# Performance work log

Measured on AMD Instinct MI355X. Metric: run time of the kernel, lower is better.

## Reference

```python
import jax, jax.numpy as jnp
import numpy as np

MAX_SENTENCE = 12
HIDDEN = 256
INPUT = 18 * 300
NEG = -9999999.0


def _lstm(xs, Wih, Whh, bih, bhh):
    # xs: [T, B, I] -> hs: [T, B, H] (torch LSTM gate order i,f,g,o)
    B = xs.shape[1]
    H = Whh.shape[1]

    def step(carry, x):
        h, c = carry
        g = x @ Wih.T + h @ Whh.T + bih + bhh
        i, f, gg, o = jnp.split(g, 4, axis=-1)
        c = jax.nn.sigmoid(f) * c + jax.nn.sigmoid(i) * jnp.tanh(gg)
        h = jax.nn.sigmoid(o) * jnp.tanh(c)
        return (h, c), h

    init = (jnp.zeros((B, H), xs.dtype), jnp.zeros((B, H), xs.dtype))
    _, hs = jax.lax.scan(step, init, xs)
    return hs


def setup_inputs() -> dict:
    key = jax.random.key(0)
    ks = jax.random.split(key, 16)
    s = 0.05
    return {
        "x": jax.random.normal(ks[0], (512, MAX_SENTENCE, INPUT), jnp.float32),
        "Wih_f": jax.random.normal(ks[1], (4 * HIDDEN, INPUT), jnp.float32) * s,
        "Whh_f": jax.random.normal(ks[2], (4 * HIDDEN, HIDDEN), jnp.float32) * s,
        "bih_f": jax.random.normal(ks[3], (4 * HIDDEN,), jnp.float32) * s,
        "bhh_f": jax.random.normal(ks[4], (4 * HIDDEN,), jnp.float32) * s,
        "Wih_b": jax.random.normal(ks[5], (4 * HIDDEN, INPUT), jnp.float32) * s,
        "Whh_b": jax.random.normal(ks[6], (4 * HIDDEN, HIDDEN), jnp.float32) * s,
        "bih_b": jax.random.normal(ks[7], (4 * HIDDEN,), jnp.float32) * s,
        "bhh_b": jax.random.normal(ks[8], (4 * HIDDEN,), jnp.float32) * s,
        "enc_W": jax.random.normal(ks[9], (50, 2 * HIDDEN), jnp.float32) * s,
        "enc_b": jax.random.normal(ks[10], (50,), jnp.float32) * s,
        "wfc_W": jax.random.normal(ks[11], (1, 100), jnp.float32) * s,
        "wfc_b": jax.random.normal(ks[12], (1,), jnp.float32) * s,
        "fc_W": jax.random.normal(ks[13], (2, MAX_SENTENCE), jnp.float32) * s,
        "fc_b": jax.random.normal(ks[14], (2,), jnp.float32) * s,
    }


def reference(x, Wih_f, Whh_f, bih_f, bhh_f, Wih_b, Whh_b, bih_b, bhh_b,
              enc_W, enc_b, wfc_W, wfc_b, fc_W, fc_b):
    # Bidirectional LSTM over the document axis (seq-first, batch = MAX_SENTENCE)
    hf = _lstm(x, Wih_f, Whh_f, bih_f, bhh_f)                       # [D, S, H]
    hb = jnp.flip(_lstm(jnp.flip(x, 0), Wih_b, Whh_b, bih_b, bhh_b), 0)
    H = jnp.concatenate([hf, hb], axis=-1)                           # [D, S, 2H]

    # Sentence encoder: Linear(2H,50) + LeakyReLU (dropout = identity, eval)
    enc = jax.nn.leaky_relu(H @ enc_W.T + enc_b, 0.01)               # [D, S, 50]

    # Pairwise affinity Wij[d,i,j] = w_fc(concat(enc_i, enc_j)); split-weight trick
    w1, w2 = wfc_W[0, :50], wfc_W[0, 50:]
    a = enc @ w1                                                     # [D, S]
    b = enc @ w2                                                     # [D, S]
    Wij = a[:, :, None] + b[:, None, :] + wfc_b[0]                   # [D, S, S]
    eye = jnp.eye(MAX_SENTENCE, dtype=bool)
    Wij = jnp.where(eye, NEG, Wij)

    # Core sentence: argmax over off-diagonal row sums
    rowsum = jnp.sum(jnp.where(eye, 0.0, Wij), axis=-1)              # [D, S]
    core = jnp.argmax(rowsum, axis=-1)                               # [D]

    # Cosine similarity of each sentence to the core sentence -> rank scores
    Hn = H / (jnp.linalg.norm(H, axis=-1, keepdims=True) + 1e-12)
    core_vec = jnp.take_along_axis(Hn, core[:, None, None], axis=1)  # [D, 1, 2H]
    sim = jnp.sum(Hn * core_vec, axis=-1)                            # [D, S]
    order = jnp.argsort(-sim, axis=-1)
    ranks = jnp.argsort(order, axis=-1)
    rank_score = 1.0 - ranks.astype(H.dtype) / MAX_SENTENCE          # [D, S]

    # Row-scaled affinities, zero diagonal for aggregation
    Wmask = jnp.where(eye, 0.0, Wij) * rank_score[:, :, None]        # [D, S, S]

    # Two rounds of weighted neighbor aggregation
    emb = H
    for _ in range(2):
        emb = emb + jnp.einsum('dij,djh->dih', Wmask, emb)

    doc = jnp.mean(emb, axis=-1)                                     # [D, S]
    return doc @ fc_W.T + fc_b                                       # [D, 2]
```

## Files before the change

### kernel.cpp

```cpp
#include <hip/hip_runtime.h>
#include <hip/hip_bf16.h>
#include <hip/hip_fp16.h>


typedef _Float16 h8 __attribute__((ext_vector_type(8)));
typedef _Float16 h2 __attribute__((ext_vector_type(2)));
typedef float f4 __attribute__((ext_vector_type(4)));

#define SEQ 512
#define NL 12
#define KIN 5400
#define KP 5408
#define NG 2048
#define MROWS 6144

__device__ __forceinline__ unsigned int pk2(float a, float b){
  h2 v; v[0] = (_Float16)a; v[1] = (_Float16)b;
  return __builtin_bit_cast(unsigned int, v);
}
__device__ __forceinline__ float dot2u(unsigned int h, unsigned int w, float acc){
  return __builtin_amdgcn_fdot2(__builtin_bit_cast(h2, h), __builtin_bit_cast(h2, w), acc, false);
}
__device__ __forceinline__ float sigm(float x){ return 1.f/(1.f + __expf(-x)); }
__device__ __forceinline__ float tanhx(float x){ return 1.f - 2.f/(__expf(2.f*x) + 1.f); }

__global__ void cvt_x(const float* __restrict__ x, _Float16* __restrict__ xh){
  int idx = blockIdx.x * 256 + threadIdx.x;
  int row = idx / KP, col = idx - row * KP;
  float v = (col < KIN) ? x[(size_t)row * KIN + col] : 0.f;
  xh[idx] = (_Float16)v;
}

__global__ void cvt_w(const float* __restrict__ wf, const float* __restrict__ wb,
                      _Float16* __restrict__ wh){
  int idx = blockIdx.x * 256 + threadIdx.x;
  int row = idx / KP, col = idx - row * KP;
  float v = 0.f;
  if (col < KIN)
    v = (row < 1024) ? wf[(size_t)row * KIN + col] : wb[(size_t)(row - 1024) * KIN + col];
  wh[idx] = (_Float16)v;
}

__global__ __launch_bounds__(256) void gemm_in(
    const _Float16* __restrict__ A, const _Float16* __restrict__ B, _Float16* __restrict__ G,
    const float* __restrict__ bif, const float* __restrict__ bhf,
    const float* __restrict__ bib, const float* __restrict__ bhb){
  __shared__ _Float16 As[128 * 40];
  __shared__ _Float16 Bs[128 * 40];
  int tid = threadIdx.x;
  int bm = blockIdx.x % 48, bn = blockIdx.x / 48;
  int wid = tid >> 6, ln = tid & 63;
  int wm = wid & 1, wn = wid >> 1;
  int l15 = ln & 15, q = ln >> 4;
  int i0 = tid, i1 = tid + 256;
  int r0 = i0 >> 2, c0 = i0 & 3, r1 = i1 >> 2, c1 = i1 & 3;
  const size_t a0 = (size_t)(bm*128 + r0) * KP + c0*8;
  const size_t a1 = (size_t)(bm*128 + r1) * KP + c1*8;
  const size_t b0 = (size_t)(bn*128 + r0) * KP + c0*8;
  const size_t b1 = (size_t)(bn*128 + r1) * KP + c1*8;
  f4 acc[4][4] = {};
  for (int kk = 0; kk < 169; ++kk){
    int k0 = kk * 32;
    uint4 va0 = *(const uint4*)(A + a0 + k0);
    uint4 va1 = *(const uint4*)(A + a1 + k0);
    uint4 vb0 = *(const uint4*)(B + b0 + k0);
    uint4 vb1 = *(const uint4*)(B + b1 + k0);
    __syncthreads();
    *(uint4*)(As + r0*40 + c0*8) = va0;
    *(uint4*)(As + r1*40 + c1*8) = va1;
    *(uint4*)(Bs + r0*40 + c0*8) = vb0;
    *(uint4*)(Bs + r1*40 + c1*8) = vb1;
    __syncthreads();
    h8 af[4], bfr[4];
    #pragma unroll
    for (int mt = 0; mt < 4; ++mt)
      af[mt] = *(const h8*)(As + (wm*64 + mt*16 + l15)*40 + q*8);
    #pragma unroll
    for (int nt = 0; nt < 4; ++nt)
      bfr[nt] = *(const h8*)(Bs + (wn*64 + nt*16 + l15)*40 + q*8);
    #pragma unroll
    for (int mt = 0; mt < 4; ++mt)
      #pragma unroll
      for (int nt = 0; nt < 4; ++nt)
        acc[mt][nt] = __builtin_amdgcn_mfma_f32_16x16x32_f16(af[mt], bfr[nt], acc[mt][nt], 0, 0, 0);
  }
  float bias[4];
  #pragma unroll
  for (int nt = 0; nt < 4; ++nt){
    int col = bn*128 + wn*64 + nt*16 + l15;
    bias[nt] = (col < 1024) ? (bif[col] + bhf[col]) : (bib[col-1024] + bhb[col-1024]);
  }
  #pragma unroll
  for (int mt = 0; mt < 4; ++mt)
    #pragma unroll
    for (int nt = 0; nt < 4; ++nt)
      #pragma unroll
      for (int r = 0; r < 4; ++r){
        int row = bm*128 + wm*64 + mt*16 + q*4 + r;
        int col = bn*128 + wn*64 + nt*16 + l15;
        G[(size_t)row * NG + col] = (_Float16)(acc[mt][nt][r] + bias[nt]);
      }
}

__global__ __launch_bounds__(512, 2) void lstm_rec(
    const float* __restrict__ Whhf, const float* __restrict__ Whhb,
    const _Float16* __restrict__ G, float* __restrict__ Hout){
  __shared__ unsigned int tailw[12][1024];
  __shared__ unsigned int hlds[128];
  __shared__ float fg[256], og[256];
  int b = blockIdx.x;
  int dir = b / 12, lane = b - dir * 12;
  int t = threadIdx.x;
  const float* Whh = dir ? Whhb : Whhf;
  int r0 = t, r1 = t + 512;
  unsigned int wa[116], wb[116];
  #pragma unroll
  for (int c = 0; c < 128; ++c){
    float2 v0 = *(const float2*)(Whh + (size_t)r0 * 256 + 2*c);
    float2 v1 = *(const float2*)(Whh + (size_t)r1 * 256 + 2*c);
    unsigned int u0 = pk2(v0.x, v0.y);
    unsigned int u1 = pk2(v1.x, v1.y);
    if (c < 116){ wa[c] = u0; wb[c] = u1; }
    else { tailw[c - 116][r0] = u0; tailw[c - 116][r1] = u1; }
  }
  if (t < 128) hlds[t] = 0u;
  float cst = 0.f;
  __syncthreads();
  for (int it = 0; it < SEQ; ++it){
    int s = dir ? (SEQ - 1 - it) : it;
    const _Float16* gp = G + (size_t)(s*NL + lane) * NG + dir * 1024;
    float ga = (float)gp[r0];
    float gb = (float)gp[r1];
    float acc0 = 0.f, acc1 = 0.f;
    #pragma unroll
    for (int c4 = 0; c4 < 29; ++c4){
      uint4 hq = *(const uint4*)&hlds[c4*4];
      unsigned int ha[4] = {hq.x, hq.y, hq.z, hq.w};
      #pragma unroll
      for (int j = 0; j < 4; ++j){
        acc0 = dot2u(ha[j], wa[c4*4 + j], acc0);
        acc1 = dot2u(ha[j], wb[c4*4 + j], acc1);
      }
    }
    #pragma unroll
    for (int c4 = 0; c4 < 3; ++c4){
      uint4 hq = *(const uint4*)&hlds[116 + c4*4];
      unsigned int ha[4] = {hq.x, hq.y, hq.z, hq.w};
      #pragma unroll
      for (int j = 0; j < 4; ++j){
        int cc = c4*4 + j;
        acc0 = dot2u(ha[j], tailw[cc][r0], acc0);
        acc1 = dot2u(ha[j], tailw[cc][r1], acc1);
      }
    }
    acc0 += ga; acc1 += gb;
    __syncthreads();
    if (t >= 256){ fg[t - 256] = acc0; og[t - 256] = acc1; }
    __syncthreads();
    if (t < 256){
      float iv = acc0, gv = acc1, fv = fg[t], ov = og[t];
      cst = sigm(fv)*cst + sigm(iv)*tanhx(gv);
      float hv = sigm(ov)*tanhx(cst);
      ((_Float16*)hlds)[t] = (_Float16)hv;
      Hout[(size_t)(s*NL + lane)*512 + dir*256 + t] = hv;
    }
    __syncthreads();
  }
}

__global__ __launch_bounds__(256) void epilogue(
    const float* __restrict__ H, const float* __restrict__ encW, const float* __restrict__ encB,
    const float* __restrict__ wfcW, const float* __restrict__ wfcB,
    const float* __restrict__ fcW, const float* __restrict__ fcB, float* __restrict__ out){
  __shared__ float B0[12][516];
  __shared__ float B1[12][516];
  __shared__ float encl[12][52];
  __shared__ float part[12][16];
  __shared__ float av[12], bv[12], nrm[12], simv[12], rsv[12], docv[12];
  __shared__ float Wm[12][12];
  __shared__ int corei;
  int d = blockIdx.x, t = threadIdx.x;
  const float* Hd = H + (size_t)d * NL * 512;
  for (int idx = t; idx < NL * 128; idx += 256){
    int i = idx >> 7, h4 = (idx & 127) * 4;
    *(f4*)(&B0[i][h4]) = *(const f4*)(Hd + i*512 + h4);
  }
  __syncthreads();
  for (int idx = t; idx < 600; idx += 256){
    int i = idx % 12, e = idx / 12;
    float s = encB[e];
    const float* w = encW + e * 512;
    for (int h = 0; h < 512; ++h) s += B0[i][h] * w[h];
    encl[i][e] = (s >= 0.f) ? s : 0.01f * s;
  }
  __syncthreads();
  if (t < 12){
    float sa = 0.f, sb = 0.f;
    for (int e = 0; e < 50; ++e){ sa += encl[t][e]*wfcW[e]; sb += encl[t][e]*wfcW[50 + e]; }
    av[t] = sa; bv[t] = sb;
  }
  __syncthreads();
  if (t < 192){
    int i = t >> 4, sl = t & 15;
    float s = 0.f;
    for (int h = sl*32; h < sl*32 + 32; ++h){ float v = B0[i][h]; s += v*v; }
    part[i][sl] = s;
  }
  if (t == 192){
    float wbv = wfcB[0];
    float best = -1e30f; int bi = 0;
    for (int i = 0; i < 12; ++i){
      float rs = 0.f;
      for (int j = 0; j < 12; ++j) if (j != i) rs += av[i] + bv[j] + wbv;
      if (rs > best){ best = rs; bi = i; }
    }
    corei = bi;
  }
  __syncthreads();
  if (t < 12){
    float s = 0.f; for (int l = 0; l < 16; ++l) s += part[t][l];
    nrm[t] = sqrtf(s) + 1e-12f;
  }
  __syncthreads();
  if (t < 192){
    int i = t >> 4, sl = t & 15, cc = corei;
    float s = 0.f;
    for (int h = sl*32; h < sl*32 + 32; ++h) s += B0[i][h] * B0[cc][h];
    part[i][sl] = s;
  }
  __syncthreads();
  if (t < 12){
    float s = 0.f; for (int l = 0; l < 16; ++l) s += part[t][l];
    simv[t] = s / (nrm[t] * nrm[corei]);
  }
  __syncthreads();
  if (t < 12){
    int rk = 0; float st = simv[t];
    for (int j = 0; j < 12; ++j){
      float sj = simv[j];
      rk += (sj > st) || (sj == st && j < t);
    }
    rsv[t] = 1.f - (float)rk / 12.f;
  }
  __syncthreads();
  if (t < 144){
    int i = t / 12, j = t - (t / 12) * 12;
    Wm[i][j] = (i == j) ? 0.f : (av[i] + bv[j] + wfcB[0]) * rsv[i];
  }
  __syncthreads();
  for (int h = t; h < 512; h += 256){
    float e[12];
    #pragma unroll
    for (int j = 0; j < 12; ++j) e[j] = B0[j][h];
    #pragma unroll
    for (int i = 0; i < 12; ++i){
      float s = e[i];
      #pragma unroll
      for (int j = 0; j < 12; ++j) s += Wm[i][j] * e[j];
      B1[i][h] = s;
    }
  }
  __syncthreads();
  for (int h = t; h < 512; h += 256){
    float e[12];
    #pragma unroll
    for (int j = 0; j < 12; ++j) e[j] = B1[j][h];
    #pragma unroll
    for (int i = 0; i < 12; ++i){
      float s = e[i];
      #pragma unroll
      for (int j = 0; j < 12; ++j) s += Wm[i][j] * e[j];
      B0[i][h] = s;
    }
  }
  __syncthreads();
  if (t < 192){
    int i = t >> 4, sl = t & 15;
    float s = 0.f;
    for (int h = sl*32; h < sl*32 + 32; ++h) s += B0[i][h];
    part[i][sl] = s;
  }
  __syncthreads();
  if (t < 12){
    float s = 0.f; for (int l = 0; l < 16; ++l) s += part[t][l];
    docv[t] = s / 512.f;
  }
  __syncthreads();
  if (t < 2){
    float s = fcB[t];
    for (int i = 0; i < 12; ++i) s += docv[i] * fcW[t*12 + i];
    out[d*2 + t] = s;
  }
}

extern "C" void kernel_launch(void* const* d_in, const int* in_sizes, int n_in,
                              void* d_out, int out_size, void* d_ws, size_t ws_size,
                              hipStream_t stream){
  const float* x    = (const float*)d_in[0];
  const float* Wihf = (const float*)d_in[1];
  const float* Whhf = (const float*)d_in[2];
  const float* bihf = (const float*)d_in[3];
  const float* bhhf = (const float*)d_in[4];
  const float* Wihb = (const float*)d_in[5];
  const float* Whhb = (const float*)d_in[6];
  const float* bihb = (const float*)d_in[7];
  const float* bhhb = (const float*)d_in[8];
  const float* encW = (const float*)d_in[9];
  const float* encB = (const float*)d_in[10];
  const float* wfcW = (const float*)d_in[11];
  const float* wfcB = (const float*)d_in[12];
  const float* fcW  = (const float*)d_in[13];
  const float* fcB  = (const float*)d_in[14];
  float* out = (float*)d_out;
  char* ws = (char*)d_ws;
  _Float16* xh = (_Float16*)(ws);
  _Float16* wh = (_Float16*)(ws + 66453504);
  _Float16* G  = (_Float16*)(ws + 88604672);
  float* H = (float*)(ws);

  cvt_x<<<129792, 256, 0, stream>>>(x, xh);
  cvt_w<<<43264, 256, 0, stream>>>(Wihf, Wihb, wh);
  gemm_in<<<768, 256, 0, stream>>>(xh, wh, G, bihf, bhhf, bihb, bhhb);
  lstm_rec<<<24, 512, 0, stream>>>(Whhf, Whhb, G, H);
  epilogue<<<512, 256, 0, stream>>>(H, encW, encB, wfcW, wfcB, fcW, fcB, out);
}
```

Baseline: 1.673 ms.

## Vectorize conversions, use direct global-to-LDS loads, and streamline LSTM gate math

```diff
diff --git a/kernel.cpp b/kernel.cpp
--- a/kernel.cpp
+++ b/kernel.cpp
@@ -5,6 +5,7 @@
 
 typedef _Float16 h8 __attribute__((ext_vector_type(8)));
 typedef _Float16 h2 __attribute__((ext_vector_type(2)));
+typedef _Float16 h4 __attribute__((ext_vector_type(4)));
 typedef float f4 __attribute__((ext_vector_type(4)));
 
 #define SEQ 512
@@ -24,65 +25,75 @@
 __device__ __forceinline__ float sigm(float x){ return 1.f/(1.f + __expf(-x)); }
 __device__ __forceinline__ float tanhx(float x){ return 1.f - 2.f/(__expf(2.f*x) + 1.f); }
 
+__device__ __forceinline__ void gload16(const void* g, void* l){
+  __builtin_amdgcn_global_load_lds((const __attribute__((address_space(1))) void*)g,
+                                   (__attribute__((address_space(3))) void*)l, 16, 0, 0);
+}
+
 __global__ void cvt_x(const float* __restrict__ x, _Float16* __restrict__ xh){
   int idx = blockIdx.x * 256 + threadIdx.x;
-  int row = idx / KP, col = idx - row * KP;
-  float v = (col < KIN) ? x[(size_t)row * KIN + col] : 0.f;
-  xh[idx] = (_Float16)v;
+  int row = idx / 1352, c4 = idx - row * 1352;
+  h4 o = {};
+  if (c4 < 1350){
+    f4 v = *(const f4*)(x + (size_t)row * KIN + c4 * 4);
+    o[0] = (_Float16)v.x; o[1] = (_Float16)v.y; o[2] = (_Float16)v.z; o[3] = (_Float16)v.w;
+  }
+  *(h4*)(xh + (size_t)row * KP + c4 * 4) = o;
 }
 
 __global__ void cvt_w(const float* __restrict__ wf, const float* __restrict__ wb,
                       _Float16* __restrict__ wh){
   int idx = blockIdx.x * 256 + threadIdx.x;
-  int row = idx / KP, col = idx - row * KP;
-  float v = 0.f;
-  if (col < KIN)
-    v = (row < 1024) ? wf[(size_t)row * KIN + col] : wb[(size_t)(row - 1024) * KIN + col];
-  wh[idx] = (_Float16)v;
+  int row = idx / 1352, c4 = idx - row * 1352;
+  h4 o = {};
+  if (c4 < 1350){
+    const float* src = (row < 1024) ? (wf + (size_t)row * KIN) : (wb + (size_t)(row - 1024) * KIN);
+    f4 v = *(const f4*)(src + c4 * 4);
+    o[0] = (_Float16)v.x; o[1] = (_Float16)v.y; o[2] = (_Float16)v.z; o[3] = (_Float16)v.w;
+  }
+  *(h4*)(wh + (size_t)row * KP + c4 * 4) = o;
 }
 
 __global__ __launch_bounds__(256) void gemm_in(
     const _Float16* __restrict__ A, const _Float16* __restrict__ B, _Float16* __restrict__ G,
     const float* __restrict__ bif, const float* __restrict__ bhf,
     const float* __restrict__ bib, const float* __restrict__ bhb){
-  __shared__ _Float16 As[128 * 40];
-  __shared__ _Float16 Bs[128 * 40];
+  __shared__ _Float16 As[128 * 32];
+  __shared__ _Float16 Bs[128 * 32];
   int tid = threadIdx.x;
   int bm = blockIdx.x % 48, bn = blockIdx.x / 48;
   int wid = tid >> 6, ln = tid & 63;
   int wm = wid & 1, wn = wid >> 1;
   int l15 = ln & 15, q = ln >> 4;
-  int i0 = tid, i1 = tid + 256;
-  int r0 = i0 >> 2, c0 = i0 & 3, r1 = i1 >> 2, c1 = i1 & 3;
-  const size_t a0 = (size_t)(bm*128 + r0) * KP + c0*8;
-  const size_t a1 = (size_t)(bm*128 + r1) * KP + c1*8;
-  const size_t b0 = (size_t)(bn*128 + r0) * KP + c0*8;
-  const size_t b1 = (size_t)(bn*128 + r1) * KP + c1*8;
+  int srow = wid * 16 + (ln >> 2);
+  int scol = (ln & 3) * 8;
+  const _Float16* a0 = A + (size_t)(bm * 128 + srow) * KP + scol;
+  const _Float16* a1 = a0 + (size_t)64 * KP;
+  const _Float16* b0 = B + (size_t)(bn * 128 + srow) * KP + scol;
+  const _Float16* b1 = b0 + (size_t)64 * KP;
+  char* AsB = (char*)As + wid * 1024;
+  char* BsB = (char*)Bs + wid * 1024;
   f4 acc[4][4] = {};
   for (int kk = 0; kk < 169; ++kk){
     int k0 = kk * 32;
-    uint4 va0 = *(const uint4*)(A + a0 + k0);
-    uint4 va1 = *(const uint4*)(A + a1 + k0);
-    uint4 vb0 = *(const uint4*)(B + b0 + k0);
-    uint4 vb1 = *(const uint4*)(B + b1 + k0);
-    __syncthreads();
-    *(uint4*)(As + r0*40 + c0*8) = va0;
-    *(uint4*)(As + r1*40 + c1*8) = va1;
-    *(uint4*)(Bs + r0*40 + c0*8) = vb0;
-    *(uint4*)(Bs + r1*40 + c1*8) = vb1;
+    gload16(a0 + k0, AsB);
+    gload16(a1 + k0, AsB + 4096);
+    gload16(b0 + k0, BsB);
+    gload16(b1 + k0, BsB + 4096);
     __syncthreads();
     h8 af[4], bfr[4];
     #pragma unroll
     for (int mt = 0; mt < 4; ++mt)
-      af[mt] = *(const h8*)(As + (wm*64 + mt*16 + l15)*40 + q*8);
+      af[mt] = *(const h8*)(As + (wm*64 + mt*16 + l15)*32 + q*8);
     #pragma unroll
     for (int nt = 0; nt < 4; ++nt)
-      bfr[nt] = *(const h8*)(Bs + (wn*64 + nt*16 + l15)*40 + q*8);
+      bfr[nt] = *(const h8*)(Bs + (wn*64 + nt*16 + l15)*32 + q*8);
     #pragma unroll
     for (int mt = 0; mt < 4; ++mt)
       #pragma unroll
       for (int nt = 0; nt < 4; ++nt)
         acc[mt][nt] = __builtin_amdgcn_mfma_f32_16x16x32_f16(af[mt], bfr[nt], acc[mt][nt], 0, 0, 0);
+    __syncthreads();
   }
   float bias[4];
   #pragma unroll
@@ -105,7 +116,7 @@
 __global__ __launch_bounds__(512, 2) void lstm_rec(
     const float* __restrict__ Whhf, const float* __restrict__ Whhb,
     const _Float16* __restrict__ G, float* __restrict__ Hout){
-  __shared__ unsigned int tailw[12][1024];
+  __shared__ unsigned int tailT[1024][12];
   __shared__ unsigned int hlds[128];
   __shared__ float fg[256], og[256];
   int b = blockIdx.x;
@@ -121,7 +132,7 @@
     unsigned int u0 = pk2(v0.x, v0.y);
     unsigned int u1 = pk2(v1.x, v1.y);
     if (c < 116){ wa[c] = u0; wb[c] = u1; }
-    else { tailw[c - 116][r0] = u0; tailw[c - 116][r1] = u1; }
+    else { tailT[r0][c - 116] = u0; tailT[r1][c - 116] = u1; }
   }
   if (t < 128) hlds[t] = 0u;
   float cst = 0.f;
@@ -145,22 +156,25 @@
     #pragma unroll
     for (int c4 = 0; c4 < 3; ++c4){
       uint4 hq = *(const uint4*)&hlds[116 + c4*4];
+      uint4 wqa = *(const uint4*)&tailT[r0][c4*4];
+      uint4 wqb = *(const uint4*)&tailT[r1][c4*4];
       unsigned int ha[4] = {hq.x, hq.y, hq.z, hq.w};
+      unsigned int qa[4] = {wqa.x, wqa.y, wqa.z, wqa.w};
+      unsigned int qb[4] = {wqb.x, wqb.y, wqb.z, wqb.w};
       #pragma unroll
       for (int j = 0; j < 4; ++j){
-        int cc = c4*4 + j;
-        acc0 = dot2u(ha[j], tailw[cc][r0], acc0);
-        acc1 = dot2u(ha[j], tailw[cc][r1], acc1);
+        acc0 = dot2u(ha[j], qa[j], acc0);
+        acc1 = dot2u(ha[j], qb[j], acc1);
       }
     }
     acc0 += ga; acc1 += gb;
-    __syncthreads();
-    if (t >= 256){ fg[t - 256] = acc0; og[t - 256] = acc1; }
+    float si = 0.f, tg = 0.f;
+    if (t < 256){ si = sigm(acc0); tg = tanhx(acc1); }
+    else { fg[t - 256] = sigm(acc0); og[t - 256] = sigm(acc1); }
     __syncthreads();
     if (t < 256){
-      float iv = acc0, gv = acc1, fv = fg[t], ov = og[t];
-      cst = sigm(fv)*cst + sigm(iv)*tanhx(gv);
-      float hv = sigm(ov)*tanhx(cst);
+      cst = fg[t]*cst + si*tg;
+      float hv = og[t]*tanhx(cst);
       ((_Float16*)hlds)[t] = (_Float16)hv;
       Hout[(size_t)(s*NL + lane)*512 + dir*256 + t] = hv;
     }
@@ -182,8 +196,8 @@
   int d = blockIdx.x, t = threadIdx.x;
   const float* Hd = H + (size_t)d * NL * 512;
   for (int idx = t; idx < NL * 128; idx += 256){
-    int i = idx >> 7, h4 = (idx & 127) * 4;
-    *(f4*)(&B0[i][h4]) = *(const f4*)(Hd + i*512 + h4);
+    int i = idx >> 7, h4i = (idx & 127) * 4;
+    *(f4*)(&B0[i][h4i]) = *(const f4*)(Hd + i*512 + h4i);
   }
   __syncthreads();
   for (int idx = t; idx < 600; idx += 256){
@@ -318,8 +332,8 @@
   _Float16* G  = (_Float16*)(ws + 88604672);
   float* H = (float*)(ws);
 
-  cvt_x<<<129792, 256, 0, stream>>>(x, xh);
-  cvt_w<<<43264, 256, 0, stream>>>(Wihf, Wihb, wh);
+  cvt_x<<<32448, 256, 0, stream>>>(x, xh);
+  cvt_w<<<10816, 256, 0, stream>>>(Wihf, Wihb, wh);
   gemm_in<<<768, 256, 0, stream>>>(xh, wh, G, bihf, bhhf, bihb, bhhb);
   lstm_rec<<<24, 512, 0, stream>>>(Whhf, Whhb, G, H);
   epilogue<<<512, 256, 0, stream>>>(H, encW, encB, wfcW, wfcB, fcW, fcB, out);
```

After: 1.551 ms. 1.08x faster.
